# Performance work log

Hardware: AMD Instinct MI355X
Metric: run time of the kernel (lower is better)

The kernel has to match this reference:

```python
import jax, jax.numpy as jnp
import numpy as np

D_MODEL = 768
KAN_HIDDEN = 2048
NUM_CP = 16        # number of B-spline control points / coefficients per edge
DEGREE = 3         # cubic splines
RMIN, RMAX = -4.0, 4.0


def bspline_basis(x, num_cp=NUM_CP, degree=DEGREE, rmin=RMIN, rmax=RMAX):
    """Cox-de Boor B-spline basis.
    x: (N, D) -> basis: (N, D, num_cp). Uniform knots extended by `degree`
    on each side so that [rmin, rmax] has full basis support.
    """
    h = (rmax - rmin) / (num_cp - degree)
    # K = num_cp + degree + 1 knots
    knots = rmin - degree * h + jnp.arange(num_cp + degree + 1, dtype=x.dtype) * h
    xe = x[..., None]  # (N, D, 1)
    # degree-0 indicator bases: (N, D, num_cp + degree)
    b = ((xe >= knots[:-1]) & (xe < knots[1:])).astype(x.dtype)
    for d in range(1, degree + 1):
        t0 = knots[:-(d + 1)]   # t[k]
        t1 = knots[d:-1]        # t[k+d]
        t2 = knots[d + 1:]      # t[k+d+1]
        t3 = knots[1:-d]        # t[k+1]
        b = (xe - t0) / (t1 - t0) * b[..., :-1] + (t2 - xe) / (t2 - t3) * b[..., 1:]
    return b  # (N, D, num_cp)


def kan_layer(x, w):
    """x: (N, Din); w: (Dout, Din, num_cp) per-edge spline coefficients."""
    basis = bspline_basis(x)                      # (N, Din, K)
    return jnp.einsum('ndk,odk->no', basis, w)    # (N, Dout)


def setup_inputs() -> dict:
    key = jax.random.key(0)
    kx, k1, k2 = jax.random.split(key, 3)
    x = jax.random.normal(kx, (2, 2048, D_MODEL), dtype=jnp.float32)
    # spline coefficient tables, small init like nn.init scaled normal
    w1 = jax.random.normal(k1, (KAN_HIDDEN, D_MODEL, NUM_CP), dtype=jnp.float32) * (1.0 / np.sqrt(D_MODEL * NUM_CP))
    w2 = jax.random.normal(k2, (D_MODEL, KAN_HIDDEN, NUM_CP), dtype=jnp.float32) * (1.0 / np.sqrt(KAN_HIDDEN * NUM_CP))
    return {"x": x, "w1": w1, "w2": w2}


def reference(x, w1, w2):
    B, T, D = x.shape
    input_dtype = x.dtype
    h = x.reshape(B * T, D).astype(jnp.float32)
    h = kan_layer(h, w1)                # (B*T, KAN_HIDDEN)
    h = kan_layer(h, w2)                # (B*T, D_MODEL)
    h = h.astype(input_dtype)
    # dropout p=0.0 / eval mode -> identity
    return h.reshape(B, T, -1)
```

## Files before the change

### kernel.cpp

```cpp
#include <hip/hip_runtime.h>
#include <stdint.h>

typedef __attribute__((ext_vector_type(8))) short short8;
typedef __attribute__((ext_vector_type(4))) float f32x4;
typedef __attribute__((ext_vector_type(4))) int i32x4;

#define DMODEL 768
#define HID    2048
#define MROWS  4096

#define KINVH  (13.0f/8.0f)
#define KNOT0  (-4.0f - 3.0f*(8.0f/13.0f))

__device__ __forceinline__ unsigned short f2bf(float f) {
  unsigned int u = __float_as_uint(f);
  unsigned int r = (u + 0x7FFFu + ((u >> 16) & 1u)) >> 16;
  return (unsigned short)r;
}

template<int DIN>
__global__ void __launch_bounds__(256) conv_pack(const float* __restrict__ src,
                                                 unsigned short* __restrict__ dst,
                                                 int total_waves) {
  constexpr int NK2 = DIN / 2;
  int gw = blockIdx.x * 4 + (threadIdx.x >> 6);
  if (gw >= total_waves) return;
  int l   = threadIdx.x & 63;
  int cb  = gw / NK2;
  int kt2 = gw % NK2;
  int c16 = l & 15, q = l >> 4;
  int col = cb * 16 + c16;
  const float* s = src + ((size_t)col * DIN + kt2 * 2 + (q >> 1)) * 16 + (q & 1) * 8;
  float4 v0 = *(const float4*)s;
  float4 v1 = *(const float4*)(s + 4);
  short8 o;
  o[0] = (short)f2bf(v0.x); o[1] = (short)f2bf(v0.y);
  o[2] = (short)f2bf(v0.z); o[3] = (short)f2bf(v0.w);
  o[4] = (short)f2bf(v1.x); o[5] = (short)f2bf(v1.y);
  o[6] = (short)f2bf(v1.z); o[7] = (short)f2bf(v1.w);
  unsigned short* d = dst + (((size_t)cb * NK2 + kt2) * 64 + q * 16 + c16) * 8;
  *(short8*)d = o;
}

__global__ void __launch_bounds__(256) reduce2(float4* __restrict__ p, int n4) {
  int i = blockIdx.x * 256 + threadIdx.x;
  if (i >= n4) return;
  float4 a = p[i], b = p[i + n4];
  float4 r;
  r.x = a.x + b.x; r.y = a.y + b.y; r.z = a.z + b.z; r.w = a.w + b.w;
  p[i] = r;
}

__global__ void __launch_bounds__(256) reduce4(const float4* __restrict__ p,
                                               float4* __restrict__ out, int n4) {
  int i = blockIdx.x * 256 + threadIdx.x;
  if (i >= n4) return;
  float4 a = p[i], b = p[i + n4], c = p[i + 2 * n4], d = p[i + 3 * n4];
  float4 r;
  r.x = a.x + b.x + c.x + d.x;
  r.y = a.y + b.y + c.y + d.y;
  r.z = a.z + b.z + c.z + d.z;
  r.w = a.w + b.w + c.w + d.w;
  out[i] = r;
}

template<int DIN, int DOUT, int SPLITK>
__global__ void __launch_bounds__(256, 2)
kan_gemm(const float* __restrict__ X, const unsigned short* __restrict__ Wb,
         float* __restrict__ Out) {
  constexpr int BM  = 64;
  constexpr int BN  = 256;
  constexpr int NK  = (DIN * 16) / 64;
  constexpr int NK2 = DIN / 2;
  constexpr int NKS = NK / SPLITK;
  constexpr int GX  = MROWS / BM;
  constexpr int GY  = DOUT / BN;
  constexpr int CPX = (GX * GY) / 8;
  __shared__ __align__(16) char smA[BM * 128];

  const int tid  = threadIdx.x;
  const int lane = tid & 63;
  const int wid  = tid >> 6;

  const int d    = blockIdx.x + blockIdx.y * GX;
  const int lf   = (d & 7) * CPX + (d >> 3);
  const int brow = (lf % GX) * BM;
  const int bcol = (lf / GX) * BN;
  const int kt0  = blockIdx.z * NKS;
  const int kt1  = kt0 + NKS;

  f32x4 acc[4][4];
#pragma unroll
  for (int m = 0; m < 4; ++m)
#pragma unroll
    for (int n = 0; n < 4; ++n) acc[m][n] = (f32x4){0.f, 0.f, 0.f, 0.f};

  int a_base[4], a_sw[4];
#pragma unroll
  for (int m = 0; m < 4; ++m) {
    int row   = m * 16 + (lane & 15);
    a_base[m] = row * 128 + ((lane >> 4) * 16);
    a_sw[m]   = (row & 7) << 4;
  }

  const unsigned short* bp[4];
#pragma unroll
  for (int n = 0; n < 4; ++n)
    bp[n] = Wb + ((size_t)(bcol / 16 + wid * 4 + n) * NK2 + (size_t)kt0 * 2) * 512
               + lane * 8;

  const int br_ = tid >> 2;
  const int bd_ = tid & 3;
  const float* xrow = X + (size_t)(brow + br_) * DIN + bd_;

  float xcur = xrow[(size_t)kt0 * 4];
  short8 bv[2][4];
#pragma unroll
  for (int n = 0; n < 4; ++n) {
    bv[0][n] = *(const short8*)(bp[n]);
    bv[1][n] = *(const short8*)(bp[n] + 512);
    bp[n] += 1024;
  }

  for (int kt = kt0; kt < kt1; ++kt) {
    __syncthreads();

    {
      float u  = (xcur - KNOT0) * KINVH;
      float uf = floorf(u);
      int   jj = (int)uf;
      float t  = u - uf;
      float t2 = t * t, t3 = t2 * t;
      float p0 = (1.0f / 6.0f) * (1.0f - 3.0f * t + 3.0f * t2 - t3);
      float p1 = (1.0f / 6.0f) * (4.0f - 6.0f * t2 + 3.0f * t3);
      float p2 = (1.0f / 6.0f) * (1.0f + 3.0f * t + 3.0f * t2 - 3.0f * t3);
      float p3 = (1.0f / 6.0f) * t3;

      int base = br_ * 128 + bd_ * 32;
      int sw   = (br_ & 7) << 4;
      *(i32x4*)(smA + (base ^ sw))        = (i32x4){0, 0, 0, 0};
      *(i32x4*)(smA + ((base + 16) ^ sw)) = (i32x4){0, 0, 0, 0};
      unsigned short q0 = f2bf(p0), q1 = f2bf(p1), q2 = f2bf(p2), q3 = f2bf(p3);
      int k0 = jj - 3;
      if ((unsigned)(k0 + 0) < 16u) *(unsigned short*)(smA + ((base + (k0 + 0) * 2) ^ sw)) = q0;
      if ((unsigned)(k0 + 1) < 16u) *(unsigned short*)(smA + ((base + (k0 + 1) * 2) ^ sw)) = q1;
      if ((unsigned)(k0 + 2) < 16u) *(unsigned short*)(smA + ((base + (k0 + 2) * 2) ^ sw)) = q2;
      if ((unsigned)(k0 + 3) < 16u) *(unsigned short*)(smA + ((base + (k0 + 3) * 2) ^ sw)) = q3;
    }

    {
      int ktn = (kt + 1 < kt1) ? kt + 1 : kt;
      xcur = xrow[(size_t)ktn * 4];
    }

    __syncthreads();

    short8 a0[4], a1[4];
#pragma unroll
    for (int m = 0; m < 4; ++m) {
      a0[m] = *(const short8*)(smA + (a_base[m] ^ a_sw[m]));
      a1[m] = *(const short8*)(smA + ((a_base[m] + 64) ^ a_sw[m]));
    }

#pragma unroll
    for (int m = 0; m < 4; ++m)
#pragma unroll
      for (int n = 0; n < 4; ++n)
        acc[m][n] = __builtin_amdgcn_mfma_f32_16x16x32_bf16(a0[m], bv[0][n], acc[m][n], 0, 0, 0);
#pragma unroll
    for (int m = 0; m < 4; ++m)
#pragma unroll
      for (int n = 0; n < 4; ++n)
        acc[m][n] = __builtin_amdgcn_mfma_f32_16x16x32_bf16(a1[m], bv[1][n], acc[m][n], 0, 0, 0);

    if (kt + 1 < kt1) {
#pragma unroll
      for (int n = 0; n < 4; ++n) {
        bv[0][n] = *(const short8*)(bp[n]);
        bv[1][n] = *(const short8*)(bp[n] + 512);
        bp[n] += 1024;
      }
    }
  }

  float* outp = Out + (size_t)blockIdx.z * MROWS * DOUT;
#pragma unroll
  for (int m = 0; m < 4; ++m)
#pragma unroll
    for (int n = 0; n < 4; ++n)
#pragma unroll
      for (int q = 0; q < 4; ++q) {
        int grow = brow + m * 16 + (lane >> 4) * 4 + q;
        int gcol = bcol + wid * 64 + n * 16 + (lane & 15);
        outp[(size_t)grow * DOUT + gcol] = acc[m][n][q];
      }
}

extern "C" void kernel_launch(void* const* d_in, const int* in_sizes, int n_in,
                              void* d_out, int out_size, void* d_ws, size_t ws_size,
                              hipStream_t stream) {
  const float* x  = (const float*)d_in[0];
  const float* w1 = (const float*)d_in[1];
  const float* w2 = (const float*)d_in[2];
  float* out = (float*)d_out;

  char* ws = (char*)d_ws;
  unsigned short* wgb   = (unsigned short*)ws;
  float*          part1 = (float*)(ws + 50331648);
  float*          hbf   = part1;
  float*          part2 = (float*)(ws + 83886080);

  {
    const int waves = (HID / 16) * (DMODEL / 2);
    conv_pack<DMODEL><<<waves / 4, 256, 0, stream>>>(w1, wgb, waves);
  }
  kan_gemm<DMODEL, HID, 2>
      <<<dim3(MROWS / 64, HID / 256, 2), 256, 0, stream>>>(x, wgb, part1);
  const int hn4 = (MROWS * HID) / 4;
  reduce2<<<hn4 / 256, 256, 0, stream>>>((float4*)part1, hn4);

  {
    const int waves = (DMODEL / 16) * (HID / 2);
    conv_pack<HID><<<waves / 4, 256, 0, stream>>>(w2, wgb, waves);
  }
  kan_gemm<HID, DMODEL, 4>
      <<<dim3(MROWS / 64, DMODEL / 256, 4), 256, 0, stream>>>(hbf, wgb, part2);
  const int rn4 = (MROWS * DMODEL) / 4;
  reduce4<<<rn4 / 256, 256, 0, stream>>>((const float4*)part2, (float4*)out, rn4);
}
```

Measured before the change: 510.0 us.

## Double-buffer LDS basis tile and overlap basis build with MFMA

Double-buffers the shared-memory A tile so the B-spline basis for the next k-step is written to one buffer while MFMAs consume the other. This drops one of the two barriers per iteration and issues the weight register prefetch before the MFMAs. The cost is twice the LDS per block and more live registers (two weight register sets), which may affect occupancy at launch_bounds(256,2). The loop is unrolled by two and assumes an even number of k-steps per split.

```diff
diff --git a/kernel.cpp b/kernel.cpp
--- a/kernel.cpp
+++ b/kernel.cpp
@@ -76,7 +76,7 @@
   constexpr int GX  = MROWS / BM;
   constexpr int GY  = DOUT / BN;
   constexpr int CPX = (GX * GY) / 8;
-  __shared__ __align__(16) char smA[BM * 128];
+  __shared__ __align__(16) char smA[2][BM * 128];
 
   const int tid  = threadIdx.x;
   const int lane = tid & 63;
@@ -113,74 +113,84 @@
   const int bd_ = tid & 3;
   const float* xrow = X + (size_t)(brow + br_) * DIN + bd_;
 
-  float xcur = xrow[(size_t)kt0 * 4];
-  short8 bv[2][4];
+  auto BASIS = [&](float xv, char* smp) {
+    float u  = (xv - KNOT0) * KINVH;
+    float uf = floorf(u);
+    int   jj = (int)uf;
+    float t  = u - uf;
+    float t2 = t * t, t3 = t2 * t;
+    float p0 = (1.0f / 6.0f) * (1.0f - 3.0f * t + 3.0f * t2 - t3);
+    float p1 = (1.0f / 6.0f) * (4.0f - 6.0f * t2 + 3.0f * t3);
+    float p2 = (1.0f / 6.0f) * (1.0f + 3.0f * t + 3.0f * t2 - 3.0f * t3);
+    float p3 = (1.0f / 6.0f) * t3;
+
+    int base = br_ * 128 + bd_ * 32;
+    int sw   = (br_ & 7) << 4;
+    *(i32x4*)(smp + (base ^ sw))        = (i32x4){0, 0, 0, 0};
+    *(i32x4*)(smp + ((base + 16) ^ sw)) = (i32x4){0, 0, 0, 0};
+    unsigned short q0 = f2bf(p0), q1 = f2bf(p1), q2 = f2bf(p2), q3 = f2bf(p3);
+    int k0 = jj - 3;
+    if ((unsigned)(k0 + 0) < 16u) *(unsigned short*)(smp + ((base + (k0 + 0) * 2) ^ sw)) = q0;
+    if ((unsigned)(k0 + 1) < 16u) *(unsigned short*)(smp + ((base + (k0 + 1) * 2) ^ sw)) = q1;
+    if ((unsigned)(k0 + 2) < 16u) *(unsigned short*)(smp + ((base + (k0 + 2) * 2) ^ sw)) = q2;
+    if ((unsigned)(k0 + 3) < 16u) *(unsigned short*)(smp + ((base + (k0 + 3) * 2) ^ sw)) = q3;
+  };
+
+  short8 bvE[2][4], bvO[2][4];
+
 #pragma unroll
   for (int n = 0; n < 4; ++n) {
-    bv[0][n] = *(const short8*)(bp[n]);
-    bv[1][n] = *(const short8*)(bp[n] + 512);
+    bvE[0][n] = *(const short8*)(bp[n]);
+    bvE[1][n] = *(const short8*)(bp[n] + 512);
     bp[n] += 1024;
   }
-
-  for (int kt = kt0; kt < kt1; ++kt) {
-    __syncthreads();
-
-    {
-      float u  = (xcur - KNOT0) * KINVH;
-      float uf = floorf(u);
-      int   jj = (int)uf;
-      float t  = u - uf;
-      float t2 = t * t, t3 = t2 * t;
-      float p0 = (1.0f / 6.0f) * (1.0f - 3.0f * t + 3.0f * t2 - t3);
-      float p1 = (1.0f / 6.0f) * (4.0f - 6.0f * t2 + 3.0f * t3);
-      float p2 = (1.0f / 6.0f) * (1.0f + 3.0f * t + 3.0f * t2 - 3.0f * t3);
-      float p3 = (1.0f / 6.0f) * t3;
-
-      int base = br_ * 128 + bd_ * 32;
-      int sw   = (br_ & 7) << 4;
-      *(i32x4*)(smA + (base ^ sw))        = (i32x4){0, 0, 0, 0};
-      *(i32x4*)(smA + ((base + 16) ^ sw)) = (i32x4){0, 0, 0, 0};
-      unsigned short q0 = f2bf(p0), q1 = f2bf(p1), q2 = f2bf(p2), q3 = f2bf(p3);
-      int k0 = jj - 3;
-      if ((unsigned)(k0 + 0) < 16u) *(unsigned short*)(smA + ((base + (k0 + 0) * 2) ^ sw)) = q0;
-      if ((unsigned)(k0 + 1) < 16u) *(unsigned short*)(smA + ((base + (k0 + 1) * 2) ^ sw)) = q1;
-      if ((unsigned)(k0 + 2) < 16u) *(unsigned short*)(smA + ((base + (k0 + 2) * 2) ^ sw)) = q2;
-      if ((unsigned)(k0 + 3) < 16u) *(unsigned short*)(smA + ((base + (k0 + 3) * 2) ^ sw)) = q3;
+  BASIS(xrow[(size_t)kt0 * 4], &smA[0][0]);
+  float xv = xrow[(size_t)((kt0 + 1 < kt1) ? kt0 + 1 : kt0) * 4];
+  __syncthreads();
+
+  auto STEP = [&](int kt, const char* smR, char* smW,
+                  short8 (&bc)[2][4], short8 (&bn)[2][4]) {
+    const bool more = (kt + 1 < kt1);
+
+    short8 a0[4], a1[4];
+#pragma unroll
+    for (int m = 0; m < 4; ++m) {
+      a0[m] = *(const short8*)(smR + (a_base[m] ^ a_sw[m]));
+      a1[m] = *(const short8*)(smR + ((a_base[m] + 64) ^ a_sw[m]));
     }
 
-    {
-      int ktn = (kt + 1 < kt1) ? kt + 1 : kt;
-      xcur = xrow[(size_t)ktn * 4];
-    }
-
-    __syncthreads();
-
-    short8 a0[4], a1[4];
-#pragma unroll
-    for (int m = 0; m < 4; ++m) {
-      a0[m] = *(const short8*)(smA + (a_base[m] ^ a_sw[m]));
-      a1[m] = *(const short8*)(smA + ((a_base[m] + 64) ^ a_sw[m]));
-    }
-
-#pragma unroll
-    for (int m = 0; m < 4; ++m)
-#pragma unroll
-      for (int n = 0; n < 4; ++n)
-        acc[m][n] = __builtin_amdgcn_mfma_f32_16x16x32_bf16(a0[m], bv[0][n], acc[m][n], 0, 0, 0);
-#pragma unroll
-    for (int m = 0; m < 4; ++m)
-#pragma unroll
-      for (int n = 0; n < 4; ++n)
-        acc[m][n] = __builtin_amdgcn_mfma_f32_16x16x32_bf16(a1[m], bv[1][n], acc[m][n], 0, 0, 0);
-
-    if (kt + 1 < kt1) {
+    if (more) {
 #pragma unroll
       for (int n = 0; n < 4; ++n) {
-        bv[0][n] = *(const short8*)(bp[n]);
-        bv[1][n] = *(const short8*)(bp[n] + 512);
+        bn[0][n] = *(const short8*)(bp[n]);
+        bn[1][n] = *(const short8*)(bp[n] + 512);
         bp[n] += 1024;
       }
     }
+
+    int ktn = (kt + 2 < kt1) ? kt + 2 : kt1 - 1;
+    float xn = xrow[(size_t)ktn * 4];
+
+    if (more) BASIS(xv, smW);
+
+#pragma unroll
+    for (int m = 0; m < 4; ++m)
+#pragma unroll
+      for (int n = 0; n < 4; ++n)
+        acc[m][n] = __builtin_amdgcn_mfma_f32_16x16x32_bf16(a0[m], bc[0][n], acc[m][n], 0, 0, 0);
+#pragma unroll
+    for (int m = 0; m < 4; ++m)
+#pragma unroll
+      for (int n = 0; n < 4; ++n)
+        acc[m][n] = __builtin_amdgcn_mfma_f32_16x16x32_bf16(a1[m], bc[1][n], acc[m][n], 0, 0, 0);
+
+    xv = xn;
+    __syncthreads();
+  };
+
+  for (int kt = kt0; kt < kt1; kt += 2) {
+    STEP(kt,     &smA[0][0], &smA[1][0], bvE, bvO);
+    STEP(kt + 1, &smA[1][0], &smA[0][0], bvO, bvE);
   }
 
   float* outp = Out + (size_t)blockIdx.z * MROWS * DOUT;
```

New measurement: 560.2 us. +9.8%, slower.
